# Kernel optimization log

Measured on AMD Instinct MI355X. Metric: run time of the kernel, lower is better.

Reference implementation:

```python
import jax, jax.numpy as jnp
import numpy as np

B, S, D, H, P, KN = 32, 197, 768, 12, 196, 32
HD = D // H
DFF = 4 * D


def layer_norm(x, g, b, eps=1e-5):
    mu = jnp.mean(x, axis=-1, keepdims=True)
    var = jnp.var(x, axis=-1, keepdims=True)
    return (x - mu) * jax.lax.rsqrt(var + eps) * g + b


def setup_inputs() -> dict:
    key = jax.random.key(0)
    ks = jax.random.split(key, 16)
    s = 0.02
    return {
        "x": jax.random.normal(ks[0], (B, S, D), dtype=jnp.float32),
        "routes": jax.random.randint(ks[1], (P, KN), 0, P, dtype=jnp.int32),
        "qkv_w": jax.random.normal(ks[2], (D, 3 * D), dtype=jnp.float32) * s,
        "qkv_b": jnp.zeros((3 * D,), jnp.float32),
        "proj_w": jax.random.normal(ks[3], (D, D), dtype=jnp.float32) * s,
        "proj_b": jnp.zeros((D,), jnp.float32),
        "n1_g": jnp.ones((D,), jnp.float32),
        "n1_b": jnp.zeros((D,), jnp.float32),
        "n2_g": jnp.ones((D,), jnp.float32),
        "n2_b": jnp.zeros((D,), jnp.float32),
        "mlp_w1": jax.random.normal(ks[4], (D, DFF), dtype=jnp.float32) * s,
        "mlp_b1": jnp.zeros((DFF,), jnp.float32),
        "mlp_w2": jax.random.normal(ks[5], (DFF, D), dtype=jnp.float32) * s,
        "mlp_b2": jnp.zeros((D,), jnp.float32),
    }


def reference(x, routes, qkv_w, qkv_b, proj_w, proj_b, n1_g, n1_b, n2_g, n2_b,
              mlp_w1, mlp_b1, mlp_w2, mlp_b2):
    scale = HD ** -0.5
    x_norm = layer_norm(x, n1_g, n1_b)
    qkv = (x_norm @ qkv_w + qkv_b).reshape(B, S, 3, H, HD)
    qkv = jnp.transpose(qkv, (2, 0, 3, 1, 4))  # [3,B,H,S,hd]
    Q, K, V = qkv[0], qkv[1], qkv[2]

    # CLS: dense attention over all S tokens
    scores_cls = jnp.einsum('bhqd,bhkd->bhqk', Q[:, :, :1], K) * scale
    attn_cls = jax.nn.softmax(scores_cls, axis=-1)
    out_cls = jnp.einsum('bhqk,bhkd->bhqd', attn_cls, V)  # [B,H,1,hd]

    # Patches: sparse attention over k routed neighbors (shift +1 skips CLS)
    routes_shifted = routes + 1  # [P,k], indices into S
    K_g = jnp.take(K, routes_shifted, axis=2)  # [B,H,P,k,hd]
    V_g = jnp.take(V, routes_shifted, axis=2)
    scores_p = jnp.einsum('bhpd,bhpkd->bhpk', Q[:, :, 1:], K_g) * scale
    attn_p = jax.nn.softmax(scores_p, axis=-1)
    out_p = jnp.einsum('bhpk,bhpkd->bhpd', attn_p, V_g)  # [B,H,P,hd]

    out = jnp.concatenate([out_cls, out_p], axis=2)  # [B,H,S,hd]
    out = jnp.transpose(out, (0, 2, 1, 3)).reshape(B, S, D)
    out = out @ proj_w + proj_b
    x = x + out

    h = layer_norm(x, n2_g, n2_b)
    h = jax.nn.gelu(h @ mlp_w1 + mlp_b1, approximate=False)
    x = x + (h @ mlp_w2 + mlp_b2)
    return x
```

## Files before the change

kernel.cpp:

```cpp
#include <hip/hip_runtime.h>
#include <hip/hip_bf16.h>
#include <math.h>

#define B_ 32
#define S_ 197
#define D_ 768
#define H_ 12
#define P_ 196
#define KN_ 32
#define HD_ 64
#define DFF_ 3072
#define M_ (B_ * S_)

typedef __attribute__((ext_vector_type(8))) short short8;
typedef __attribute__((ext_vector_type(8))) __bf16 bf16x8;
typedef __attribute__((ext_vector_type(4))) float f32x4;
typedef __attribute__((ext_vector_type(4))) float float4v;

static __device__ __forceinline__ unsigned short f2bf(float f) {
    unsigned u = __builtin_bit_cast(unsigned, f);
    u += 0x7FFFu + ((u >> 16) & 1u);
    return (unsigned short)(u >> 16);
}
static __device__ __forceinline__ float bf2f(unsigned short s) {
    unsigned u = ((unsigned)s) << 16;
    return __builtin_bit_cast(float, u);
}

static __device__ __forceinline__ void gload_lds16(const void* g, void* l) {
    __builtin_amdgcn_global_load_lds(
        (const __attribute__((address_space(1))) unsigned int*)g,
        (__attribute__((address_space(3))) unsigned int*)l, 16, 0, 0);
}

__global__ void __launch_bounds__(256) cvt_t_kernel(const float* __restrict__ in,
        unsigned short* __restrict__ out, int K, int N) {
    __shared__ float tile[32][33];
    int nt = N >> 5;
    int bx = blockIdx.x % nt;
    int by = blockIdx.x / nt;
    int n0 = bx << 5, k0 = by << 5;
    int tx = threadIdx.x & 31, ty = threadIdx.x >> 5;
    #pragma unroll
    for (int i = 0; i < 32; i += 8)
        tile[ty + i][tx] = in[(size_t)(k0 + ty + i) * N + n0 + tx];
    __syncthreads();
    #pragma unroll
    for (int i = 0; i < 32; i += 8)
        out[(size_t)(n0 + ty + i) * K + k0 + tx] = f2bf(tile[tx][ty + i]);
}

__global__ void __launch_bounds__(256) ln_kernel(const float* __restrict__ x,
        const float* __restrict__ g, const float* __restrict__ bt,
        unsigned short* __restrict__ out) {
    int row = blockIdx.x;
    int tid = threadIdx.x;
    const float* xr = x + (size_t)row * D_;
    float v0 = xr[tid], v1 = xr[tid + 256], v2 = xr[tid + 512];
    float s = v0 + v1 + v2;
    float q = v0 * v0 + v1 * v1 + v2 * v2;
    #pragma unroll
    for (int o = 32; o >= 1; o >>= 1) {
        s += __shfl_xor(s, o);
        q += __shfl_xor(q, o);
    }
    __shared__ float red[8];
    int wave = tid >> 6, lane = tid & 63;
    if (lane == 0) { red[wave] = s; red[4 + wave] = q; }
    __syncthreads();
    float S0 = red[0] + red[1] + red[2] + red[3];
    float Q0 = red[4] + red[5] + red[6] + red[7];
    float mean = S0 * (1.0f / D_);
    float var = Q0 * (1.0f / D_) - mean * mean;
    float rstd = rsqrtf(var + 1e-5f);
    unsigned short* orow = out + (size_t)row * D_;
    orow[tid]       = f2bf((v0 - mean) * rstd * g[tid]       + bt[tid]);
    orow[tid + 256] = f2bf((v1 - mean) * rstd * g[tid + 256] + bt[tid + 256]);
    orow[tid + 512] = f2bf((v2 - mean) * rstd * g[tid + 512] + bt[tid + 512]);
}

template<int BM, int BN, int EPI>
__global__ void __launch_bounds__(256) gemm_kernel(
        const unsigned short* __restrict__ A,
        const unsigned short* __restrict__ Bt,
        const float* __restrict__ bias,
        const float* __restrict__ resid,
        void* __restrict__ outp,
        int M, int N, int K) {
    constexpr int BK = 64;
    constexpr int WM = BM / 2, WN = BN / 2;
    constexpr int MR = WM / 16, NR = WN / 16;
    constexpr int ACH = BM / 8;
    constexpr int BCH = BN / 8;
    constexpr int ASZ = BM * BK, BSZ = BN * BK;
    __shared__ short As[2 * ASZ];
    __shared__ short Bs[2 * BSZ];

    int nwg = gridDim.x;
    int orig = blockIdx.x;
    int q8 = nwg >> 3, r8 = nwg & 7;
    int xcd = orig & 7, idx = orig >> 3;
    int wg = (xcd < r8 ? xcd * (q8 + 1) : r8 * (q8 + 1) + (xcd - r8) * q8) + idx;

    int ntn = N / BN;
    int bm = (wg / ntn) * BM;
    int bn = (wg % ntn) * BN;
    int tid = threadIdx.x;
    int lane = tid & 63;
    int wave = tid >> 6;
    int wm = (wave >> 1) * WM, wn = (wave & 1) * WN;
    int lr = lane & 15;
    int lk0 = (lane >> 4) << 3;
    int crow = lane >> 3;
    int scol = (((lane & 7) ^ ((lane >> 3) & 7)) << 3);
    int rsw = (lr & 7) << 3;

    f32x4 acc[MR][NR] = {};

    auto stage = [&](int kt, int buf) {
        short* Ad = &As[buf * ASZ];
        short* Bd = &Bs[buf * BSZ];
        #pragma unroll
        for (int c = wave; c < ACH; c += 4) {
            int grow = bm + c * 8 + crow;
            if (grow >= M) grow = M - 1;
            gload_lds16(A + (size_t)grow * K + kt + scol, &Ad[c * 512]);
        }
        #pragma unroll
        for (int c = wave; c < BCH; c += 4) {
            int grow = bn + c * 8 + crow;
            gload_lds16(Bt + (size_t)grow * K + kt + scol, &Bd[c * 512]);
        }
    };

    int nt = K / BK;
    stage(0, 0);
    __syncthreads();

    for (int t = 0; t < nt; ++t) {
        int cur = t & 1;
        if (t + 1 < nt) stage((t + 1) * BK, cur ^ 1);
        const short* Ab = &As[cur * ASZ];
        const short* Bb = &Bs[cur * BSZ];
        __builtin_amdgcn_s_setprio(1);
        #pragma unroll
        for (int kk = 0; kk < 2; ++kk) {
            int lkb = lk0 + kk * 32;
            bf16x8 af[MR], bfv[NR];
            #pragma unroll
            for (int m = 0; m < MR; ++m)
                af[m] = __builtin_bit_cast(bf16x8,
                    *(const short8*)(&Ab[(wm + m * 16 + lr) * BK + (lkb ^ rsw)]));
            #pragma unroll
            for (int n = 0; n < NR; ++n)
                bfv[n] = __builtin_bit_cast(bf16x8,
                    *(const short8*)(&Bb[(wn + n * 16 + lr) * BK + (lkb ^ rsw)]));
            #pragma unroll
            for (int m = 0; m < MR; ++m)
                #pragma unroll
                for (int n = 0; n < NR; ++n)
                    acc[m][n] = __builtin_amdgcn_mfma_f32_16x16x32_bf16(
                        af[m], bfv[n], acc[m][n], 0, 0, 0);
        }
        __builtin_amdgcn_s_setprio(0);
        __syncthreads();
    }

    int r0 = (lane >> 4) << 2;
    #pragma unroll
    for (int m = 0; m < MR; ++m) {
        #pragma unroll
        for (int n = 0; n < NR; ++n) {
            int col = bn + wn + n * 16 + lr;
            #pragma unroll
            for (int r = 0; r < 4; ++r) {
                int row = bm + wm + m * 16 + r0 + r;
                if (row < M) {
                    float v = acc[m][n][r] + bias[col];
                    if (EPI == 1)
                        v = 0.5f * v * (1.0f + erff(v * 0.70710678118f));
                    if (EPI == 2) {
                        ((float*)outp)[(size_t)row * N + col] =
                            v + resid[(size_t)row * N + col];
                    } else {
                        ((unsigned short*)outp)[(size_t)row * N + col] = f2bf(v);
                    }
                }
            }
        }
    }
}

__global__ void __launch_bounds__(256) attn_patch_kernel(
        const unsigned short* __restrict__ qkv,
        const int* __restrict__ routes,
        unsigned short* __restrict__ out) {
    int wid = (blockIdx.x * 256 + threadIdx.x) >> 6;
    int lane = threadIdx.x & 63;
    int b = wid / (H_ * P_);
    int rem = wid - b * (H_ * P_);
    int h = rem / P_;
    int p = rem - h * P_;
    int ks = lane & 31, half = lane >> 5;
    int skey = routes[p * KN_ + ks] + 1;
    const unsigned short* Qrow = qkv + (size_t)(b * S_ + p + 1) * (3 * D_) + h * HD_;
    const unsigned short* Krow = qkv + (size_t)(b * S_ + skey) * (3 * D_) + D_ + h * HD_;
    float dot = 0.f;
    #pragma unroll
    for (int q = 0; q < 4; ++q) {
        short8 qv = *(const short8*)(Qrow + half * 32 + q * 8);
        short8 kv = *(const short8*)(Krow + half * 32 + q * 8);
        #pragma unroll
        for (int j = 0; j < 8; ++j)
            dot += bf2f((unsigned short)qv[j]) * bf2f((unsigned short)kv[j]);
    }
    dot += __shfl_xor(dot, 32);
    float sc = dot * 0.125f;
    float mx = sc;
    #pragma unroll
    for (int o = 16; o >= 1; o >>= 1) mx = fmaxf(mx, __shfl_xor(mx, o));
    float e = __expf(sc - mx);
    float ssum = e;
    #pragma unroll
    for (int o = 16; o >= 1; o >>= 1) ssum += __shfl_xor(ssum, o);
    float w = e / ssum;
    const unsigned short* Vb = qkv + (size_t)b * S_ * (3 * D_) + 2 * D_ + h * HD_;
    float o_acc = 0.f;
    #pragma unroll 4
    for (int k = 0; k < 32; ++k) {
        float wk = __shfl(w, k);
        int sk = __shfl(skey, k);
        o_acc += wk * bf2f(Vb[(size_t)sk * (3 * D_) + lane]);
    }
    out[(size_t)(b * S_ + p + 1) * D_ + h * HD_ + lane] = f2bf(o_acc);
}

__global__ void __launch_bounds__(256) attn_cls_kernel(
        const unsigned short* __restrict__ qkv,
        unsigned short* __restrict__ out) {
    int wid = (blockIdx.x * 256 + threadIdx.x) >> 6;
    int lane = threadIdx.x & 63;
    int b = wid / H_, h = wid - b * H_;
    int ks = lane & 31, half = lane >> 5;
    const unsigned short* base = qkv + (size_t)b * S_ * (3 * D_);
    const unsigned short* Qrow = base + h * HD_;
    short8 qv[4];
    #pragma unroll
    for (int q = 0; q < 4; ++q)
        qv[q] = *(const short8*)(Qrow + half * 32 + q * 8);
    float sc[7];
    #pragma unroll
    for (int c = 0; c < 7; ++c) {
        int key = c * 32 + ks;
        float dot = 0.f;
        if (key < S_) {
            const unsigned short* Krow =
                base + (size_t)key * (3 * D_) + D_ + h * HD_ + half * 32;
            #pragma unroll
            for (int q = 0; q < 4; ++q) {
                short8 kv = *(const short8*)(Krow + q * 8);
                #pragma unroll
                for (int j = 0; j < 8; ++j)
                    dot += bf2f((unsigned short)qv[q][j]) * bf2f((unsigned short)kv[j]);
            }
        }
        dot += __shfl_xor(dot, 32);
        sc[c] = (key < S_) ? dot * 0.125f : -1e30f;
    }
    float mx = -1e30f;
    #pragma unroll
    for (int c = 0; c < 7; ++c) mx = fmaxf(mx, sc[c]);
    #pragma unroll
    for (int o = 16; o >= 1; o >>= 1) mx = fmaxf(mx, __shfl_xor(mx, o));
    float e[7];
    float ssum = 0.f;
    #pragma unroll
    for (int c = 0; c < 7; ++c) { e[c] = __expf(sc[c] - mx); ssum += e[c]; }
    #pragma unroll
    for (int o = 16; o >= 1; o >>= 1) ssum += __shfl_xor(ssum, o);
    float inv = 1.f / ssum;
    const unsigned short* Vb = base + 2 * D_ + h * HD_;
    float o_acc = 0.f;
    for (int c = 0; c < 7; ++c) {
        for (int k = 0; k < 32; ++k) {
            int key = c * 32 + k;
            if (key < S_) {
                float wk = __shfl(e[c], k) * inv;
                o_acc += wk * bf2f(Vb[(size_t)key * (3 * D_) + lane]);
            }
        }
    }
    out[(size_t)(b * S_) * D_ + h * HD_ + lane] = f2bf(o_acc);
}

extern "C" void kernel_launch(void* const* d_in, const int* in_sizes, int n_in,
                              void* d_out, int out_size, void* d_ws, size_t ws_size,
                              hipStream_t stream) {
    const float* x      = (const float*)d_in[0];
    const int*   routes = (const int*)d_in[1];
    const float* qkv_w  = (const float*)d_in[2];
    const float* qkv_b  = (const float*)d_in[3];
    const float* proj_w = (const float*)d_in[4];
    const float* proj_b = (const float*)d_in[5];
    const float* n1_g   = (const float*)d_in[6];
    const float* n1_b   = (const float*)d_in[7];
    const float* n2_g   = (const float*)d_in[8];
    const float* n2_b   = (const float*)d_in[9];
    const float* w1     = (const float*)d_in[10];
    const float* b1     = (const float*)d_in[11];
    const float* w2     = (const float*)d_in[12];
    const float* b2     = (const float*)d_in[13];
    float* out = (float*)d_out;

    char* ws = (char*)d_ws;
    size_t off = 0;
    auto alloc = [&](size_t bytes) -> void* {
        void* p = ws + off;
        off += (bytes + 255) & ~(size_t)255;
        return p;
    };
    unsigned short* wq_bf  = (unsigned short*)alloc((size_t)D_ * 3 * D_ * 2);
    unsigned short* wp_bf  = (unsigned short*)alloc((size_t)D_ * D_ * 2);
    unsigned short* w1_bf  = (unsigned short*)alloc((size_t)D_ * DFF_ * 2);
    unsigned short* w2_bf  = (unsigned short*)alloc((size_t)DFF_ * D_ * 2);
    unsigned short* xn_bf  = (unsigned short*)alloc((size_t)M_ * D_ * 2);
    float*          x1     = (float*)alloc((size_t)M_ * D_ * 4);
    unsigned short* qkv_bf = (unsigned short*)alloc((size_t)M_ * 3 * D_ * 2);
    unsigned short* attn_bf= (unsigned short*)alloc((size_t)M_ * D_ * 2);
    unsigned short* h_bf   = qkv_bf;

    auto cvt_t = [&](const float* src, unsigned short* dst, int K, int N) {
        cvt_t_kernel<<<(N >> 5) * (K >> 5), 256, 0, stream>>>(src, dst, K, N);
    };
    cvt_t(qkv_w, wq_bf, D_, 3 * D_);
    cvt_t(proj_w, wp_bf, D_, D_);
    cvt_t(w1, w1_bf, D_, DFF_);
    cvt_t(w2, w2_bf, DFF_, D_);

    ln_kernel<<<M_, 256, 0, stream>>>(x, n1_g, n1_b, xn_bf);

    gemm_kernel<128, 128, 0><<<50 * (3 * D_ / 128), 256, 0, stream>>>(
        xn_bf, wq_bf, qkv_b, nullptr, qkv_bf, M_, 3 * D_, D_);

    attn_patch_kernel<<<(B_ * H_ * P_) / 4, 256, 0, stream>>>(qkv_bf, routes, attn_bf);
    attn_cls_kernel<<<(B_ * H_) / 4, 256, 0, stream>>>(qkv_bf, attn_bf);

    gemm_kernel<128, 64, 2><<<50 * (D_ / 64), 256, 0, stream>>>(
        attn_bf, wp_bf, proj_b, x, x1, M_, D_, D_);

    ln_kernel<<<M_, 256, 0, stream>>>(x1, n2_g, n2_b, xn_bf);

    gemm_kernel<128, 128, 1><<<50 * (DFF_ / 128), 256, 0, stream>>>(
        xn_bf, w1_bf, b1, nullptr, h_bf, M_, DFF_, D_);

    gemm_kernel<128, 64, 2><<<50 * (D_ / 64), 256, 0, stream>>>(
        h_bf, w2_bf, b2, x1, out, M_, D_, DFF_);
}
```

Measured before the change: 430.7 us.

## Add 256x256 eight-wave GEMM with phased LDS pipeline for QKV and MLP1

Measured after the change: 452.7 us. +5.1%, slower.

```diff
diff --git a/kernel.cpp b/kernel.cpp
--- a/kernel.cpp
+++ b/kernel.cpp
@@ -77,6 +77,131 @@
     orow[tid]       = f2bf((v0 - mean) * rstd * g[tid]       + bt[tid]);
     orow[tid + 256] = f2bf((v1 - mean) * rstd * g[tid + 256] + bt[tid + 256]);
     orow[tid + 512] = f2bf((v2 - mean) * rstd * g[tid + 512] + bt[tid + 512]);
+}
+
+#define DO_PHASE(X, MB, CA, RELOAD_B, CPN, ...)                               \
+  {                                                                           \
+    bf16x8 af_[4];                                                            \
+    _Pragma("unroll")                                                         \
+    for (int m_ = 0; m_ < 4; ++m_)                                            \
+      af_[m_] = __builtin_bit_cast(bf16x8, *(const short8*)&As[X][ah][((MB) * 16 + m_ * 16 + lr) * 64 + (CA)]); \
+    if (RELOAD_B) {                                                           \
+      _Pragma("unroll")                                                       \
+      for (int n_ = 0; n_ < 4; ++n_)                                          \
+        bfr[n_] = __builtin_bit_cast(bf16x8, *(const short8*)&Bs[X][bh][(boff + n_ * 16 + lr) * 64 + (CA)]); \
+    }                                                                         \
+    __VA_ARGS__;                                                              \
+    __builtin_amdgcn_s_barrier();                                             \
+    asm volatile("s_waitcnt lgkmcnt(0)" ::: "memory");                        \
+    __builtin_amdgcn_sched_barrier(0);                                        \
+    __builtin_amdgcn_s_setprio(1);                                            \
+    _Pragma("unroll")                                                         \
+    for (int m_ = 0; m_ < 4; ++m_)                                            \
+      _Pragma("unroll")                                                       \
+      for (int n_ = 0; n_ < 4; ++n_)                                          \
+        acc[(MB) + m_][n_] = __builtin_amdgcn_mfma_f32_16x16x32_bf16(         \
+            af_[m_], bfr[n_], acc[(MB) + m_][n_], 0, 0, 0);                   \
+    __builtin_amdgcn_s_setprio(0);                                            \
+    if ((CPN) == 2) asm volatile("s_waitcnt vmcnt(2)" ::: "memory");          \
+    if ((CPN) == 4) asm volatile("s_waitcnt vmcnt(4)" ::: "memory");          \
+    __builtin_amdgcn_s_barrier();                                             \
+  }
+
+template<int EPI>
+__global__ void __launch_bounds__(512, 1) gemm256_kernel(
+        const unsigned short* __restrict__ A,
+        const unsigned short* __restrict__ Bt,
+        const float* __restrict__ bias,
+        void* __restrict__ outp,
+        int M, int N, int K) {
+    __shared__ short As[2][2][8192];
+    __shared__ short Bs[2][2][8192];
+
+    int nwg = gridDim.x;
+    int orig = blockIdx.x;
+    int q8 = nwg >> 3, r8 = nwg & 7;
+    int xcd = orig & 7, idx = orig >> 3;
+    int wg = (xcd < r8 ? xcd * (q8 + 1) : r8 * (q8 + 1) + (xcd - r8) * q8) + idx;
+
+    int ntn = N >> 8;
+    int bm = (wg / ntn) << 8;
+    int bn = (wg % ntn) << 8;
+    int tid = threadIdx.x;
+    int lane = tid & 63;
+    int wave = tid >> 6;
+    int ah = wave >> 2;
+    int bh = (wave & 3) >> 1;
+    int boff = (wave & 1) * 64;
+    int lr = lane & 15;
+    int cA0 = ((lane >> 4) << 3) ^ ((lr & 7) << 3);
+    int cA1 = (32 + ((lane >> 4) << 3)) ^ ((lr & 7) << 3);
+    int scol = (((lane & 7) ^ ((lane >> 3) & 7)) << 3);
+    int srow = lane >> 3;
+
+    auto stageA = [&](int buf, int half, int kt) {
+        #pragma unroll
+        for (int cc = 0; cc < 2; ++cc) {
+            int c = wave + cc * 8;
+            int grow = bm + half * 128 + c * 8 + srow;
+            if (grow >= M) grow = M - 1;
+            gload_lds16(A + (size_t)grow * K + kt + scol, &As[buf][half][c * 512]);
+        }
+    };
+    auto stageB = [&](int buf, int half, int kt) {
+        #pragma unroll
+        for (int cc = 0; cc < 2; ++cc) {
+            int c = wave + cc * 8;
+            int grow = bn + half * 128 + c * 8 + srow;
+            gload_lds16(Bt + (size_t)grow * K + kt + scol, &Bs[buf][half][c * 512]);
+        }
+    };
+
+    f32x4 acc[8][4] = {};
+    bf16x8 bfr[4];
+
+    int nt = K >> 6;
+    int niter = nt >> 1;
+
+    stageA(0, 0, 0); stageA(0, 1, 0);
+    stageB(0, 0, 0); stageB(0, 1, 0);
+    stageB(1, 0, 64); stageB(1, 1, 64);
+    asm volatile("s_waitcnt vmcnt(4)" ::: "memory");
+    __builtin_amdgcn_s_barrier();
+
+    for (int i = 0; i < niter; ++i) {
+        int ktu = ((i << 1) + 1) << 6;
+        int kt2 = ((i << 1) + 2 < nt ? (i << 1) + 2 : (i << 1)) << 6;
+        int kt3 = ((i << 1) + 3 < nt ? (i << 1) + 3 : (i << 1) + 1) << 6;
+        DO_PHASE(0, 0, cA0, 1, -1, stageA(1, 0, ktu))
+        DO_PHASE(0, 4, cA0, 0, -1, stageA(1, 1, ktu))
+        DO_PHASE(0, 0, cA1, 1, -1, )
+        DO_PHASE(0, 4, cA1, 0,  2, stageB(0, 0, kt2))
+        DO_PHASE(1, 0, cA0, 1, -1, stageB(0, 1, kt2); stageA(0, 0, kt2))
+        DO_PHASE(1, 4, cA0, 0, -1, stageA(0, 1, kt2))
+        DO_PHASE(1, 0, cA1, 1, -1, )
+        DO_PHASE(1, 4, cA1, 0,  4, stageB(1, 0, kt3); stageB(1, 1, kt3))
+    }
+
+    int r0 = (lane >> 4) << 2;
+    int wmr = bm + ah * 128;
+    int wnc = bn + (wave & 3) * 64;
+    #pragma unroll
+    for (int m = 0; m < 8; ++m) {
+        #pragma unroll
+        for (int n = 0; n < 4; ++n) {
+            int col = wnc + n * 16 + lr;
+            #pragma unroll
+            for (int r = 0; r < 4; ++r) {
+                int row = wmr + m * 16 + r0 + r;
+                if (row < M) {
+                    float v = acc[m][n][r] + bias[col];
+                    if (EPI == 1)
+                        v = 0.5f * v * (1.0f + erff(v * 0.70710678118f));
+                    ((unsigned short*)outp)[(size_t)row * N + col] = f2bf(v);
+                }
+            }
+        }
+    }
 }
 
 template<int BM, int BN, int EPI>
@@ -339,8 +464,8 @@
 
     ln_kernel<<<M_, 256, 0, stream>>>(x, n1_g, n1_b, xn_bf);
 
-    gemm_kernel<128, 128, 0><<<50 * (3 * D_ / 128), 256, 0, stream>>>(
-        xn_bf, wq_bf, qkv_b, nullptr, qkv_bf, M_, 3 * D_, D_);
+    gemm256_kernel<0><<<25 * (3 * D_ / 256), 512, 0, stream>>>(
+        xn_bf, wq_bf, qkv_b, qkv_bf, M_, 3 * D_, D_);
 
     attn_patch_kernel<<<(B_ * H_ * P_) / 4, 256, 0, stream>>>(qkv_bf, routes, attn_bf);
     attn_cls_kernel<<<(B_ * H_) / 4, 256, 0, stream>>>(qkv_bf, attn_bf);
@@ -350,8 +475,8 @@
 
     ln_kernel<<<M_, 256, 0, stream>>>(x1, n2_g, n2_b, xn_bf);
 
-    gemm_kernel<128, 128, 1><<<50 * (DFF_ / 128), 256, 0, stream>>>(
-        xn_bf, w1_bf, b1, nullptr, h_bf, M_, DFF_, D_);
+    gemm256_kernel<1><<<25 * (DFF_ / 256), 512, 0, stream>>>(
+        xn_bf, w1_bf, b1, h_bf, M_, DFF_, D_);
 
     gemm_kernel<128, 64, 2><<<50 * (D_ / 64), 256, 0, stream>>>(
         h_bf, w2_bf, b2, x1, out, M_, D_, DFF_);
```
